# Kernel tuning notes

Hardware: AMD Instinct MI355X
Metric: run time of the kernel (lower is better)

The kernel has to match this reference:

```python
import jax, jax.numpy as jnp
import numpy as np

T, B, IN, OUT, N_MOD, K = 1024, 8, 1024, 1024, 16, 2

def setup_inputs() -> dict:
    key = jax.random.key(0)
    k1, k2, k3, k4 = jax.random.split(key, 4)
    x = jax.random.normal(k1, (T, B, IN), dtype=jnp.float32)
    selection = jax.random.randint(k2, (B, K), 0, N_MOD, dtype=jnp.int64)
    weight = jax.random.normal(k3, (N_MOD, IN, OUT), dtype=jnp.float32) * (1.0 / np.sqrt(IN))
    bias = jax.random.normal(k4, (N_MOD, OUT), dtype=jnp.float32) * 0.02
    return {"x": x, "selection": selection, "weight": weight, "bias": bias}

def reference(x, selection, weight, bias):
    # time_major=True: x is [T, B, in] -> batch-major [B, T, in]
    xb = jnp.swapaxes(x, 0, 1)
    # Gather the K selected expert weight matrices per batch row: [B, K, in, out]
    W_sel = weight[selection]
    # Equivalent to matmul(x[i], cat(weight[sel], dim=1)): [B, T, K, out]
    o = jnp.einsum('bti,bkio->btko', xb, W_sel)
    Bn, Tn, Kn, On = o.shape
    o = o.reshape(Bn, Tn, Kn * On)
    # concat_dim == 1 bias: bias[sel].view(1, -1) -> [1, K*out], broadcast over T
    o = o + bias[selection].reshape(Bn, 1, Kn * On)
    # back to time-major [T, B, K*out]
    return jnp.swapaxes(o, 0, 1)
```

## Files before the change

kernel.cpp:

```cpp
#include <hip/hip_runtime.h>

#define T_DIM 1024
#define B_DIM 8
#define IN_DIM 1024
#define OUT_DIM 1024
#define N_MODL 16
#define K_SEL 2

typedef unsigned short ushort_t;
typedef __bf16 bf16x8 __attribute__((ext_vector_type(8)));
typedef float f32x4 __attribute__((ext_vector_type(4)));

__device__ __forceinline__ unsigned int f2bf2(float lo, float hi) {
  union { float f; unsigned int u; } a, b; a.f = lo; b.f = hi;
  unsigned int ra = (a.u + 0x7fffu + ((a.u >> 16) & 1u)) >> 16;
  unsigned int rb = (b.u + 0x7fffu + ((b.u >> 16) & 1u)) >> 16;
  return ra | (rb << 16);
}

__device__ __forceinline__ void async_g2l(const void* g, void* l) {
  __builtin_amdgcn_global_load_lds(
      (const __attribute__((address_space(1))) unsigned int*)g,
      (__attribute__((address_space(3))) unsigned int*)l,
      16, 0, 0);
}

__device__ __forceinline__ int read_sel(const int* __restrict__ s, int g) {
  bool i64 = true;
#pragma unroll
  for (int j = 0; j < 8; ++j) i64 &= (s[2 * j + 1] == 0);
  return i64 ? s[2 * g] : s[g];
}

__global__ __launch_bounds__(256) void convert_kernel(const float* __restrict__ x,
                                                      const float* __restrict__ w,
                                                      const int* __restrict__ selp,
                                                      ushort_t* __restrict__ xb,
                                                      ushort_t* __restrict__ wt) {
  __shared__ ushort_t tb[128 * 128];
  const int bid = blockIdx.x;
  if (bid >= 1024) {
    const int i = (bid - 1024) * 256 + threadIdx.x;
    const float4* s = (const float4*)x;
    float4 a = s[i * 2], b = s[i * 2 + 1];
    uint4 o;
    o.x = f2bf2(a.x, a.y); o.y = f2bf2(a.z, a.w);
    o.z = f2bf2(b.x, b.y); o.w = f2bf2(b.z, b.w);
    ((uint4*)xb)[i] = o;
    return;
  }
  const int m = bid >> 6;
  bool used = false;
#pragma unroll
  for (int g = 0; g < B_DIM * K_SEL; ++g) used |= (read_sel(selp, g) == m);
  if (!used) return;

  const int i0 = ((bid >> 3) & 7) * 128;
  const int o0 = (bid & 7) * 128;
  const float* src = w + ((size_t)(m * IN_DIM + i0)) * OUT_DIM + o0;

  const int o4 = (threadIdx.x & 31) * 4;
  const int ib = threadIdx.x >> 5;
#pragma unroll
  for (int p = 0; p < 16; ++p) {
    const int i = ib + p * 8;
    float4 v = *(const float4*)(src + (size_t)i * OUT_DIM + o4);
    const int osw = o4 ^ (((i >> 3) & 15) << 2);
    uint2 d2; d2.x = f2bf2(v.x, v.y); d2.y = f2bf2(v.z, v.w);
    *(uint2*)(tb + i * 128 + osw) = d2;
  }
  __syncthreads();

  ushort_t* dst = wt + ((size_t)(m * OUT_DIM + o0)) * IN_DIM + i0;
  const int il = (threadIdx.x & 15) * 8;
  const int ob = threadIdx.x >> 4;
  const int q2 = ((il >> 3) & 15) << 2;
#pragma unroll
  for (int p = 0; p < 8; ++p) {
    const int o = ob + p * 16;
    const int osw = o ^ q2;
    uint4 d;
    unsigned int u[8];
#pragma unroll
    for (int j = 0; j < 8; ++j) u[j] = tb[(il + j) * 128 + osw];
    d.x = u[0] | (u[1] << 16); d.y = u[2] | (u[3] << 16);
    d.z = u[4] | (u[5] << 16); d.w = u[6] | (u[7] << 16);
    *(uint4*)(dst + (size_t)o * IN_DIM + il) = d;
  }
}

__global__ __launch_bounds__(256, 2) void mlgemm_kernel(const ushort_t* __restrict__ xb,
                                                        const ushort_t* __restrict__ wt,
                                                        const int* __restrict__ selp,
                                                        const float* __restrict__ bias,
                                                        float* __restrict__ out) {
  __shared__ ushort_t As[128 * 64];
  __shared__ ushort_t Bs[2][128 * 64];

  const int lin = blockIdx.x;
  const int b = lin & 7;
  const int mtile = (lin >> 3) & 7;
  const int ntile = lin >> 6;
  const int e0 = read_sel(selp, 2 * b);
  const int e1 = read_sel(selp, 2 * b + 1);

  const ushort_t* A  = xb + (size_t)b * IN_DIM;
  const ushort_t* B0 = wt + (size_t)e0 * OUT_DIM * IN_DIM;
  const ushort_t* B1 = wt + (size_t)e1 * OUT_DIM * IN_DIM;

  const int m0 = mtile * 128;
  const int n0 = ntile * 128;

  const int lane = threadIdx.x & 63;
  const int wv = threadIdx.x >> 6;

  const int srow = lane >> 3;
  const int sx = (((lane & 7) ^ (srow & 7)) << 3);
  const ushort_t* Ab  = A  + (size_t)(m0 + srow) * (B_DIM * IN_DIM) + sx;
  const ushort_t* Bb0 = B0 + (size_t)(n0 + srow) * IN_DIM + sx;
  const ushort_t* Bb1 = B1 + (size_t)(n0 + srow) * IN_DIM + sx;

  const int frow = lane & 15;
  const int quad = lane >> 4;
  const int cbase = ((quad ^ (frow & 7)) << 3);
  const int wrow = (wv & 1) * 64;
  const int wcol = (wv >> 1) * 64;
  const ushort_t* Ard  = As    + (wrow + frow) * 64;
  const ushort_t* Brd0 = Bs[0] + (wcol + frow) * 64;
  const ushort_t* Brd1 = Bs[1] + (wcol + frow) * 64;

  f32x4 acc0[4][4] = {};
  f32x4 acc1[4][4] = {};

  for (int k0 = 0; k0 < IN_DIM; k0 += 64) {
#pragma unroll
    for (int c = 0; c < 4; ++c) {
      const int j = wv * 4 + c;
      async_g2l(Ab  + (size_t)(8 * j) * (B_DIM * IN_DIM) + k0, As + j * 512);
      async_g2l(Bb0 + (size_t)(8 * j) * IN_DIM + k0, Bs[0] + j * 512);
      async_g2l(Bb1 + (size_t)(8 * j) * IN_DIM + k0, Bs[1] + j * 512);
    }
    __syncthreads();
#pragma unroll
    for (int kk = 0; kk < 64; kk += 32) {
      const int coff = cbase ^ kk;
      bf16x8 af[4], bf0[4], bf1[4];
#pragma unroll
      for (int i = 0; i < 4; ++i) {
        af[i]  = *(const bf16x8*)(Ard  + i * 16 * 64 + coff);
        bf0[i] = *(const bf16x8*)(Brd0 + i * 16 * 64 + coff);
        bf1[i] = *(const bf16x8*)(Brd1 + i * 16 * 64 + coff);
      }
#pragma unroll
      for (int mt = 0; mt < 4; ++mt)
#pragma unroll
        for (int nt = 0; nt < 4; ++nt) {
          acc0[mt][nt] = __builtin_amdgcn_mfma_f32_16x16x32_bf16(af[mt], bf0[nt],
                                                                 acc0[mt][nt], 0, 0, 0);
          acc1[mt][nt] = __builtin_amdgcn_mfma_f32_16x16x32_bf16(af[mt], bf1[nt],
                                                                 acc1[mt][nt], 0, 0, 0);
        }
    }
    __syncthreads();
  }

  const int orow0 = m0 + wrow + quad * 4;
  const int ocol0 = n0 + wcol + frow;
  const float* bp0 = bias + (size_t)e0 * OUT_DIM;
  const float* bp1 = bias + (size_t)e1 * OUT_DIM;
  float bv0[4], bv1[4];
#pragma unroll
  for (int nt = 0; nt < 4; ++nt) {
    bv0[nt] = bp0[ocol0 + nt * 16];
    bv1[nt] = bp1[ocol0 + nt * 16];
  }
  float* C0 = out + (size_t)b * (K_SEL * OUT_DIM);
  float* C1 = C0 + OUT_DIM;
#pragma unroll
  for (int mt = 0; mt < 4; ++mt) {
#pragma unroll
    for (int r = 0; r < 4; ++r) {
      const size_t rowoff = (size_t)(orow0 + mt * 16 + r) * (B_DIM * K_SEL * OUT_DIM);
#pragma unroll
      for (int nt = 0; nt < 4; ++nt) {
        C0[rowoff + ocol0 + nt * 16] = acc0[mt][nt][r] + bv0[nt];
        C1[rowoff + ocol0 + nt * 16] = acc1[mt][nt][r] + bv1[nt];
      }
    }
  }
}

extern "C" void kernel_launch(void* const* d_in, const int* in_sizes, int n_in,
                              void* d_out, int out_size, void* d_ws, size_t ws_size,
                              hipStream_t stream) {
  const float* x    = (const float*)d_in[0];
  const int*   sel  = (const int*)d_in[1];
  const float* w    = (const float*)d_in[2];
  const float* bias = (const float*)d_in[3];
  float* out = (float*)d_out;

  ushort_t* xb = (ushort_t*)d_ws;
  ushort_t* wt = (ushort_t*)((char*)d_ws +
                             (size_t)T_DIM * B_DIM * IN_DIM * 2);

  convert_kernel<<<dim3(1024 + T_DIM * B_DIM * IN_DIM / 8 / 256), 256, 0, stream>>>(
      x, w, sel, xb, wt);
  mlgemm_kernel<<<dim3(8 * 8 * B_DIM), 256, 0, stream>>>(xb, wt, sel, bias, out);
}
```

Measured before the change: 177.0 us.

## Rewrite expert GEMM with 256x256 tiles, double-buffered async LDS loads and MFMA priority

The grouped GEMM moves from 128x128 tiles covering both experts with 256 threads to 256x256 single-expert tiles with 512 threads (8 waves). Global-to-LDS loads are double-buffered and interleaved with MFMA phases using explicit s_barrier, waitcnt and sched_barrier, and s_setprio raises MFMA priority. The aim is to hide load latency and improve LDS reuse per tile. The grid shrinks to 256 blocks and LDS grows to 128KB per block, which lowers occupancy and may leave some compute units idle.

After: 177.4 us. No clear change (+0.2%).

```diff
diff --git a/kernel.cpp b/kernel.cpp
--- a/kernel.cpp
+++ b/kernel.cpp
@@ -89,103 +89,185 @@
   }
 }
 
-__global__ __launch_bounds__(256, 2) void mlgemm_kernel(const ushort_t* __restrict__ xb,
+#define MFMA16 __builtin_amdgcn_mfma_f32_16x16x32_bf16
+
+template<bool SN, bool SN2, bool WV, bool W0>
+__device__ __forceinline__ void gemm_step(
+    int s, ushort_t* curA, ushort_t* curB, ushort_t* nxtA, ushort_t* nxtB,
+    const ushort_t* aS, const ushort_t* bS, int stLds,
+    int ardo, int brdo, int cb, f32x4 (&acc)[8][4]) {
+  const int k0n  = (s + 1) << 6;
+  const int k0n2 = (s + 2) << 6;
+  const ushort_t* Ard = curA + ardo;
+  const ushort_t* Brd = curB + brdo;
+  bf16x8 bf0[4], bf1[4], af[4];
+
+#pragma unroll
+  for (int i = 0; i < 4; ++i) af[i] = *(const bf16x8*)(Ard + i * 1024 + cb);
+#pragma unroll
+  for (int n = 0; n < 4; ++n) bf0[n] = *(const bf16x8*)(Brd + n * 1024 + cb);
+  if (SN) async_g2l(aS + (size_t)64 * 8192 + k0n, nxtA + 4096 + stLds);
+  __builtin_amdgcn_sched_barrier(0);
+  __builtin_amdgcn_s_barrier();
+  asm volatile("s_waitcnt lgkmcnt(0)" ::: "memory");
+  __builtin_amdgcn_sched_barrier(0);
+  __builtin_amdgcn_s_setprio(1);
+#pragma unroll
+  for (int i = 0; i < 4; ++i)
+#pragma unroll
+    for (int n = 0; n < 4; ++n)
+      acc[i][n] = MFMA16(af[i], bf0[n], acc[i][n], 0, 0, 0);
+  __builtin_amdgcn_s_setprio(0);
+  __builtin_amdgcn_sched_barrier(0);
+  __builtin_amdgcn_s_barrier();
+
+#pragma unroll
+  for (int i = 0; i < 4; ++i) af[i] = *(const bf16x8*)(Ard + i * 1024 + (cb ^ 32));
+#pragma unroll
+  for (int n = 0; n < 4; ++n) bf1[n] = *(const bf16x8*)(Brd + n * 1024 + (cb ^ 32));
+  if (SN) async_g2l(aS + (size_t)192 * 8192 + k0n, nxtA + 3 * 4096 + stLds);
+  __builtin_amdgcn_sched_barrier(0);
+  __builtin_amdgcn_s_barrier();
+  asm volatile("s_waitcnt lgkmcnt(0)" ::: "memory");
+  __builtin_amdgcn_sched_barrier(0);
+  __builtin_amdgcn_s_setprio(1);
+#pragma unroll
+  for (int i = 0; i < 4; ++i)
+#pragma unroll
+    for (int n = 0; n < 4; ++n)
+      acc[i][n] = MFMA16(af[i], bf1[n], acc[i][n], 0, 0, 0);
+  __builtin_amdgcn_s_setprio(0);
+  __builtin_amdgcn_sched_barrier(0);
+  __builtin_amdgcn_s_barrier();
+
+#pragma unroll
+  for (int i = 0; i < 4; ++i) af[i] = *(const bf16x8*)(Ard + (4 + i) * 1024 + cb);
+  if (SN2) {
+    async_g2l(aS + k0n2,                      curA + stLds);
+    async_g2l(aS + (size_t)128 * 8192 + k0n2, curA + 2 * 4096 + stLds);
+    async_g2l(bS + k0n2,                      curB + stLds);
+    async_g2l(bS + (size_t)64 * 1024 + k0n2,  curB + 4096 + stLds);
+  }
+  __builtin_amdgcn_sched_barrier(0);
+  __builtin_amdgcn_s_barrier();
+  asm volatile("s_waitcnt lgkmcnt(0)" ::: "memory");
+  __builtin_amdgcn_sched_barrier(0);
+  __builtin_amdgcn_s_setprio(1);
+#pragma unroll
+  for (int i = 0; i < 4; ++i)
+#pragma unroll
+    for (int n = 0; n < 4; ++n)
+      acc[4 + i][n] = MFMA16(af[i], bf0[n], acc[4 + i][n], 0, 0, 0);
+  __builtin_amdgcn_s_setprio(0);
+  __builtin_amdgcn_sched_barrier(0);
+  __builtin_amdgcn_s_barrier();
+
+#pragma unroll
+  for (int i = 0; i < 4; ++i) af[i] = *(const bf16x8*)(Ard + (4 + i) * 1024 + (cb ^ 32));
+  if (SN2) {
+    async_g2l(bS + (size_t)128 * 1024 + k0n2, curB + 2 * 4096 + stLds);
+    async_g2l(bS + (size_t)192 * 1024 + k0n2, curB + 3 * 4096 + stLds);
+  }
+  __builtin_amdgcn_sched_barrier(0);
+  __builtin_amdgcn_s_barrier();
+  asm volatile("s_waitcnt lgkmcnt(0)" ::: "memory");
+  __builtin_amdgcn_sched_barrier(0);
+  __builtin_amdgcn_s_setprio(1);
+#pragma unroll
+  for (int i = 0; i < 4; ++i)
+#pragma unroll
+    for (int n = 0; n < 4; ++n)
+      acc[4 + i][n] = MFMA16(af[i], bf1[n], acc[4 + i][n], 0, 0, 0);
+  __builtin_amdgcn_s_setprio(0);
+  if (WV) {
+    if (W0) asm volatile("s_waitcnt vmcnt(0)" ::: "memory");
+    else    asm volatile("s_waitcnt vmcnt(6)" ::: "memory");
+  }
+  __builtin_amdgcn_sched_barrier(0);
+  __builtin_amdgcn_s_barrier();
+}
+
+__global__ __launch_bounds__(512, 2) void mlgemm_kernel(const ushort_t* __restrict__ xb,
                                                         const ushort_t* __restrict__ wt,
                                                         const int* __restrict__ selp,
                                                         const float* __restrict__ bias,
                                                         float* __restrict__ out) {
-  __shared__ ushort_t As[128 * 64];
-  __shared__ ushort_t Bs[2][128 * 64];
+  __shared__ ushort_t As[2][256 * 64];
+  __shared__ ushort_t Bs[2][256 * 64];
 
   const int lin = blockIdx.x;
   const int b = lin & 7;
-  const int mtile = (lin >> 3) & 7;
-  const int ntile = lin >> 6;
-  const int e0 = read_sel(selp, 2 * b);
-  const int e1 = read_sel(selp, 2 * b + 1);
-
-  const ushort_t* A  = xb + (size_t)b * IN_DIM;
-  const ushort_t* B0 = wt + (size_t)e0 * OUT_DIM * IN_DIM;
-  const ushort_t* B1 = wt + (size_t)e1 * OUT_DIM * IN_DIM;
-
-  const int m0 = mtile * 128;
-  const int n0 = ntile * 128;
-
-  const int lane = threadIdx.x & 63;
-  const int wv = threadIdx.x >> 6;
-
-  const int srow = lane >> 3;
-  const int sx = (((lane & 7) ^ (srow & 7)) << 3);
-  const ushort_t* Ab  = A  + (size_t)(m0 + srow) * (B_DIM * IN_DIM) + sx;
-  const ushort_t* Bb0 = B0 + (size_t)(n0 + srow) * IN_DIM + sx;
-  const ushort_t* Bb1 = B1 + (size_t)(n0 + srow) * IN_DIM + sx;
-
+  const int mtile = (lin >> 3) & 3;
+  const int ntile = lin >> 5;
+  const int e = (ntile < 4) ? read_sel(selp, 2 * b) : read_sel(selp, 2 * b + 1);
+  const int n0e = (ntile & 3) * 256;
+  const int m0 = mtile * 256;
+
+  const int tid = threadIdx.x;
+  const int lane = tid & 63;
+  const int wv = tid >> 6;
+  const int wm = wv >> 2;
+  const int wn = wv & 3;
   const int frow = lane & 15;
   const int quad = lane >> 4;
-  const int cbase = ((quad ^ (frow & 7)) << 3);
-  const int wrow = (wv & 1) * 64;
-  const int wcol = (wv >> 1) * 64;
-  const ushort_t* Ard  = As    + (wrow + frow) * 64;
-  const ushort_t* Brd0 = Bs[0] + (wcol + frow) * 64;
-  const ushort_t* Brd1 = Bs[1] + (wcol + frow) * 64;
-
-  f32x4 acc0[4][4] = {};
-  f32x4 acc1[4][4] = {};
-
-  for (int k0 = 0; k0 < IN_DIM; k0 += 64) {
-#pragma unroll
-    for (int c = 0; c < 4; ++c) {
-      const int j = wv * 4 + c;
-      async_g2l(Ab  + (size_t)(8 * j) * (B_DIM * IN_DIM) + k0, As + j * 512);
-      async_g2l(Bb0 + (size_t)(8 * j) * IN_DIM + k0, Bs[0] + j * 512);
-      async_g2l(Bb1 + (size_t)(8 * j) * IN_DIM + k0, Bs[1] + j * 512);
-    }
-    __syncthreads();
-#pragma unroll
-    for (int kk = 0; kk < 64; kk += 32) {
-      const int coff = cbase ^ kk;
-      bf16x8 af[4], bf0[4], bf1[4];
-#pragma unroll
-      for (int i = 0; i < 4; ++i) {
-        af[i]  = *(const bf16x8*)(Ard  + i * 16 * 64 + coff);
-        bf0[i] = *(const bf16x8*)(Brd0 + i * 16 * 64 + coff);
-        bf1[i] = *(const bf16x8*)(Brd1 + i * 16 * 64 + coff);
-      }
-#pragma unroll
-      for (int mt = 0; mt < 4; ++mt)
-#pragma unroll
-        for (int nt = 0; nt < 4; ++nt) {
-          acc0[mt][nt] = __builtin_amdgcn_mfma_f32_16x16x32_bf16(af[mt], bf0[nt],
-                                                                 acc0[mt][nt], 0, 0, 0);
-          acc1[mt][nt] = __builtin_amdgcn_mfma_f32_16x16x32_bf16(af[mt], bf1[nt],
-                                                                 acc1[mt][nt], 0, 0, 0);
-        }
-    }
-    __syncthreads();
-  }
-
-  const int orow0 = m0 + wrow + quad * 4;
-  const int ocol0 = n0 + wcol + frow;
-  const float* bp0 = bias + (size_t)e0 * OUT_DIM;
-  const float* bp1 = bias + (size_t)e1 * OUT_DIM;
-  float bv0[4], bv1[4];
-#pragma unroll
-  for (int nt = 0; nt < 4; ++nt) {
-    bv0[nt] = bp0[ocol0 + nt * 16];
-    bv1[nt] = bp1[ocol0 + nt * 16];
-  }
-  float* C0 = out + (size_t)b * (K_SEL * OUT_DIM);
-  float* C1 = C0 + OUT_DIM;
-#pragma unroll
-  for (int mt = 0; mt < 4; ++mt) {
+  const int cb = ((quad ^ (lane & 7)) << 3);
+
+  const int sr = tid >> 3;
+  const int sch = (tid & 7) ^ (sr & 7);
+  const ushort_t* aS = xb + (size_t)(m0 + sr) * (B_DIM * IN_DIM) + b * IN_DIM + sch * 8;
+  const ushort_t* bS = wt + ((size_t)(e * OUT_DIM + n0e + sr)) * IN_DIM + sch * 8;
+  const int stLds = wv * 512;
+
+  const int ardo = (wm * 128 + frow) * 64;
+  const int brdo = (wn * 64 + frow) * 64;
+
+  f32x4 acc[8][4] = {};
+
+  async_g2l(aS,                           As[0] + stLds);
+  async_g2l(aS + (size_t)64 * 8192,       As[0] + 4096 + stLds);
+  async_g2l(aS + (size_t)128 * 8192,      As[0] + 2 * 4096 + stLds);
+  async_g2l(aS + (size_t)192 * 8192,      As[0] + 3 * 4096 + stLds);
+  async_g2l(bS,                           Bs[0] + stLds);
+  async_g2l(bS + (size_t)64 * 1024,       Bs[0] + 4096 + stLds);
+  async_g2l(bS + (size_t)128 * 1024,      Bs[0] + 2 * 4096 + stLds);
+  async_g2l(bS + (size_t)192 * 1024,      Bs[0] + 3 * 4096 + stLds);
+  __builtin_amdgcn_sched_barrier(0);
+  async_g2l(aS + 64,                      As[1] + stLds);
+  async_g2l(aS + (size_t)128 * 8192 + 64, As[1] + 2 * 4096 + stLds);
+  async_g2l(bS + 64,                      Bs[1] + stLds);
+  async_g2l(bS + (size_t)64 * 1024 + 64,  Bs[1] + 4096 + stLds);
+  async_g2l(bS + (size_t)128 * 1024 + 64, Bs[1] + 2 * 4096 + stLds);
+  async_g2l(bS + (size_t)192 * 1024 + 64, Bs[1] + 3 * 4096 + stLds);
+  __builtin_amdgcn_sched_barrier(0);
+  asm volatile("s_waitcnt vmcnt(6)" ::: "memory");
+  __builtin_amdgcn_s_barrier();
+  __builtin_amdgcn_sched_barrier(0);
+
+  for (int s = 0; s < 14; s += 2) {
+    gemm_step<true, true, true, false>(s,     As[0], Bs[0], As[1], Bs[1],
+                                       aS, bS, stLds, ardo, brdo, cb, acc);
+    gemm_step<true, true, true, false>(s + 1, As[1], Bs[1], As[0], Bs[0],
+                                       aS, bS, stLds, ardo, brdo, cb, acc);
+  }
+  gemm_step<true, false, true, true>(14, As[0], Bs[0], As[1], Bs[1],
+                                     aS, bS, stLds, ardo, brdo, cb, acc);
+  gemm_step<false, false, false, false>(15, As[1], Bs[1], As[0], Bs[0],
+                                        aS, bS, stLds, ardo, brdo, cb, acc);
+
+  const float* bp = bias + (size_t)e * OUT_DIM + n0e + wn * 64 + frow;
+  float bv[4];
+#pragma unroll
+  for (int n = 0; n < 4; ++n) bv[n] = bp[n * 16];
+  const int colb = ntile * 256 + wn * 64 + frow;
+  const int trow = m0 + wm * 128 + quad * 4;
+  float* ob = out + (size_t)b * (K_SEL * OUT_DIM) + colb;
+#pragma unroll
+  for (int m = 0; m < 8; ++m) {
 #pragma unroll
     for (int r = 0; r < 4; ++r) {
-      const size_t rowoff = (size_t)(orow0 + mt * 16 + r) * (B_DIM * K_SEL * OUT_DIM);
-#pragma unroll
-      for (int nt = 0; nt < 4; ++nt) {
-        C0[rowoff + ocol0 + nt * 16] = acc0[mt][nt][r] + bv0[nt];
-        C1[rowoff + ocol0 + nt * 16] = acc1[mt][nt][r] + bv1[nt];
-      }
+      float* orow = ob + (size_t)(trow + m * 16 + r) * (B_DIM * K_SEL * OUT_DIM);
+#pragma unroll
+      for (int n = 0; n < 4; ++n) orow[n * 16] = acc[m][n][r] + bv[n];
     }
   }
 }
@@ -205,5 +287,5 @@
 
   convert_kernel<<<dim3(1024 + T_DIM * B_DIM * IN_DIM / 8 / 256), 256, 0, stream>>>(
       x, w, sel, xb, wt);
-  mlgemm_kernel<<<dim3(8 * 8 * B_DIM), 256, 0, stream>>>(xb, wt, sel, bias, out);
-}
+  mlgemm_kernel<<<dim3(8 * 4 * 8), 512, 0, stream>>>(xb, wt, sel, bias, out);
+}
```

## Triple-buffer LDS tiles with async prefetch two K-steps ahead

Applied to the files above, without the earlier changes.

Replaces the single-buffered 64-wide K loop with a three-stage ring of 32-wide LDS buffers. Global-to-LDS loads are issued two steps ahead, with manual vmcnt waits and one barrier per step, so memory latency overlaps the MFMA work. The LDS swizzle and load mapping are reworked for the narrower 32-element rows. In exchange there are more barriers and more manual waitcnt logic, and the changed swizzle could cause LDS bank conflicts.

Measured after the change: 179.5 us. Within noise of the previous version (+1.4%).

```diff
diff --git a/kernel.cpp b/kernel.cpp
--- a/kernel.cpp
+++ b/kernel.cpp
@@ -89,13 +89,15 @@
   }
 }
 
+#define MFMA16 __builtin_amdgcn_mfma_f32_16x16x32_bf16
+
 __global__ __launch_bounds__(256, 2) void mlgemm_kernel(const ushort_t* __restrict__ xb,
                                                         const ushort_t* __restrict__ wt,
                                                         const int* __restrict__ selp,
                                                         const float* __restrict__ bias,
                                                         float* __restrict__ out) {
-  __shared__ ushort_t As[128 * 64];
-  __shared__ ushort_t Bs[2][128 * 64];
+  __shared__ ushort_t As[3][128 * 32];
+  __shared__ ushort_t Bs[3][2][128 * 32];
 
   const int lin = blockIdx.x;
   const int b = lin & 7;
@@ -103,65 +105,94 @@
   const int ntile = lin >> 6;
   const int e0 = read_sel(selp, 2 * b);
   const int e1 = read_sel(selp, 2 * b + 1);
-
-  const ushort_t* A  = xb + (size_t)b * IN_DIM;
-  const ushort_t* B0 = wt + (size_t)e0 * OUT_DIM * IN_DIM;
-  const ushort_t* B1 = wt + (size_t)e1 * OUT_DIM * IN_DIM;
-
   const int m0 = mtile * 128;
   const int n0 = ntile * 128;
 
-  const int lane = threadIdx.x & 63;
-  const int wv = threadIdx.x >> 6;
-
-  const int srow = lane >> 3;
-  const int sx = (((lane & 7) ^ (srow & 7)) << 3);
-  const ushort_t* Ab  = A  + (size_t)(m0 + srow) * (B_DIM * IN_DIM) + sx;
-  const ushort_t* Bb0 = B0 + (size_t)(n0 + srow) * IN_DIM + sx;
-  const ushort_t* Bb1 = B1 + (size_t)(n0 + srow) * IN_DIM + sx;
+  const int tid = threadIdx.x;
+  const int lane = tid & 63;
+  const int wv = tid >> 6;
+
+  const int re = lane >> 2;
+  const int cl = (lane & 3) ^ ((lane >> 3) & 3);
+  const int j0 = wv * 2, j1 = j0 + 1;
+  const ushort_t* aP0 = xb + (size_t)(m0 + j0 * 16 + re) * (B_DIM * IN_DIM)
+                           + b * IN_DIM + cl * 8;
+  const ushort_t* aP1 = aP0 + (size_t)16 * (B_DIM * IN_DIM);
+  const ushort_t* b0P0 = wt + ((size_t)(e0 * OUT_DIM + n0 + j0 * 16 + re)) * IN_DIM
+                            + cl * 8;
+  const ushort_t* b0P1 = b0P0 + (size_t)16 * IN_DIM;
+  const ushort_t* b1P0 = wt + ((size_t)(e1 * OUT_DIM + n0 + j0 * 16 + re)) * IN_DIM
+                            + cl * 8;
+  const ushort_t* b1P1 = b1P0 + (size_t)16 * IN_DIM;
+  const int jo0 = j0 * 512, jo1 = j1 * 512;
 
   const int frow = lane & 15;
   const int quad = lane >> 4;
-  const int cbase = ((quad ^ (frow & 7)) << 3);
+  const int cp = quad ^ ((frow >> 1) & 3);
   const int wrow = (wv & 1) * 64;
   const int wcol = (wv >> 1) * 64;
-  const ushort_t* Ard  = As    + (wrow + frow) * 64;
-  const ushort_t* Brd0 = Bs[0] + (wcol + frow) * 64;
-  const ushort_t* Brd1 = Bs[1] + (wcol + frow) * 64;
+  const int rdoA = (wrow + frow) * 32 + cp * 8;
+  const int rdoB = (wcol + frow) * 32 + cp * 8;
 
   f32x4 acc0[4][4] = {};
   f32x4 acc1[4][4] = {};
 
-  for (int k0 = 0; k0 < IN_DIM; k0 += 64) {
-#pragma unroll
-    for (int c = 0; c < 4; ++c) {
-      const int j = wv * 4 + c;
-      async_g2l(Ab  + (size_t)(8 * j) * (B_DIM * IN_DIM) + k0, As + j * 512);
-      async_g2l(Bb0 + (size_t)(8 * j) * IN_DIM + k0, Bs[0] + j * 512);
-      async_g2l(Bb1 + (size_t)(8 * j) * IN_DIM + k0, Bs[1] + j * 512);
-    }
-    __syncthreads();
-#pragma unroll
-    for (int kk = 0; kk < 64; kk += 32) {
-      const int coff = cbase ^ kk;
-      bf16x8 af[4], bf0[4], bf1[4];
-#pragma unroll
-      for (int i = 0; i < 4; ++i) {
-        af[i]  = *(const bf16x8*)(Ard  + i * 16 * 64 + coff);
-        bf0[i] = *(const bf16x8*)(Brd0 + i * 16 * 64 + coff);
-        bf1[i] = *(const bf16x8*)(Brd1 + i * 16 * 64 + coff);
+#pragma unroll
+  for (int k = 0; k < 2; ++k) {
+    const int k0 = k * 32;
+    async_g2l(aP0 + k0,  As[k] + jo0);
+    async_g2l(aP1 + k0,  As[k] + jo1);
+    async_g2l(b0P0 + k0, Bs[k][0] + jo0);
+    async_g2l(b0P1 + k0, Bs[k][0] + jo1);
+    async_g2l(b1P0 + k0, Bs[k][1] + jo0);
+    async_g2l(b1P1 + k0, Bs[k][1] + jo1);
+  }
+  asm volatile("s_waitcnt vmcnt(6)" ::: "memory");
+  __builtin_amdgcn_sched_barrier(0);
+  __builtin_amdgcn_s_barrier();
+  __builtin_amdgcn_sched_barrier(0);
+
+#pragma unroll
+  for (int t = 0; t < 32; ++t) {
+    const int cur = t % 3;
+    const int nxt = (t + 2) % 3;
+    if (t < 30) {
+      const int k0n = (t + 2) * 32;
+      async_g2l(aP0 + k0n,  As[nxt] + jo0);
+      async_g2l(aP1 + k0n,  As[nxt] + jo1);
+      async_g2l(b0P0 + k0n, Bs[nxt][0] + jo0);
+      async_g2l(b0P1 + k0n, Bs[nxt][0] + jo1);
+      async_g2l(b1P0 + k0n, Bs[nxt][1] + jo0);
+      async_g2l(b1P1 + k0n, Bs[nxt][1] + jo1);
+      __builtin_amdgcn_sched_barrier(0);
+    }
+    const ushort_t* Ard  = As[cur] + rdoA;
+    const ushort_t* Brd0 = Bs[cur][0] + rdoB;
+    const ushort_t* Brd1 = Bs[cur][1] + rdoB;
+    bf16x8 af[4], bf0[4], bf1[4];
+#pragma unroll
+    for (int i = 0; i < 4; ++i) {
+      af[i]  = *(const bf16x8*)(Ard  + i * 512);
+      bf0[i] = *(const bf16x8*)(Brd0 + i * 512);
+      bf1[i] = *(const bf16x8*)(Brd1 + i * 512);
+    }
+#pragma unroll
+    for (int mt = 0; mt < 4; ++mt)
+#pragma unroll
+      for (int nt = 0; nt < 4; ++nt) {
+        acc0[mt][nt] = MFMA16(af[mt], bf0[nt], acc0[mt][nt], 0, 0, 0);
+        acc1[mt][nt] = MFMA16(af[mt], bf1[nt], acc1[mt][nt], 0, 0, 0);
       }
-#pragma unroll
-      for (int mt = 0; mt < 4; ++mt)
-#pragma unroll
-        for (int nt = 0; nt < 4; ++nt) {
-          acc0[mt][nt] = __builtin_amdgcn_mfma_f32_16x16x32_bf16(af[mt], bf0[nt],
-                                                                 acc0[mt][nt], 0, 0, 0);
-          acc1[mt][nt] = __builtin_amdgcn_mfma_f32_16x16x32_bf16(af[mt], bf1[nt],
-                                                                 acc1[mt][nt], 0, 0, 0);
-        }
-    }
-    __syncthreads();
+    if (t < 29) {
+      asm volatile("s_waitcnt vmcnt(6)" ::: "memory");
+    } else if (t < 31) {
+      asm volatile("s_waitcnt vmcnt(0)" ::: "memory");
+    }
+    if (t < 31) {
+      __builtin_amdgcn_sched_barrier(0);
+      __builtin_amdgcn_s_barrier();
+      __builtin_amdgcn_sched_barrier(0);
+    }
   }
 
   const int orow0 = m0 + wrow + quad * 4;
```

## Double-buffer B tiles and prefetch next k-step during MFMA compute

Applied to the files above, without the earlier changes.

Restructures the GEMM main loop into a software pipeline: the two expert weight tiles are double-buffered in LDS and the next k-step's B loads are issued before computing the current one. The A tile stays single-buffered and is reloaded right after its fragments are read into registers, behind a barrier. Manual waitcnt and sched_barrier calls control ordering. The goal is to hide global-to-LDS latency behind MFMA work, at the cost of 16KB more LDS (48KB per block), which may affect occupancy at 2 blocks per CU.

New measurement: 174.8 us. No clear change (-1.3%).

```diff
diff --git a/kernel.cpp b/kernel.cpp
--- a/kernel.cpp
+++ b/kernel.cpp
@@ -89,13 +89,89 @@
   }
 }
 
+#define MFMA16 __builtin_amdgcn_mfma_f32_16x16x32_bf16
+
+template<bool LAST>
+__device__ __forceinline__ void gstep(
+    int t, ushort_t* As,
+    const ushort_t* curB0, const ushort_t* curB1,
+    ushort_t* nxtB0, ushort_t* nxtB1,
+    const ushort_t* Ab, const ushort_t* Bb0, const ushort_t* Bb1,
+    int wv, int ardo, int brdo, int cb,
+    f32x4 (&acc0)[4][4], f32x4 (&acc1)[4][4]) {
+  const int k1 = (t + 1) * 64;
+  if (!LAST) {
+#pragma unroll
+    for (int c = 0; c < 4; ++c) {
+      const int j = wv * 4 + c;
+      async_g2l(Bb0 + (size_t)8 * j * IN_DIM + k1, nxtB0 + j * 512);
+      async_g2l(Bb1 + (size_t)8 * j * IN_DIM + k1, nxtB1 + j * 512);
+    }
+    __builtin_amdgcn_sched_barrier(0);
+  }
+  bf16x8 af0[4], af1[4];
+  const ushort_t* Ard = As + ardo;
+#pragma unroll
+  for (int i = 0; i < 4; ++i) {
+    af0[i] = *(const bf16x8*)(Ard + i * 1024 + cb);
+    af1[i] = *(const bf16x8*)(Ard + i * 1024 + (cb ^ 32));
+  }
+  if (!LAST) {
+    __builtin_amdgcn_sched_barrier(0);
+    asm volatile("s_waitcnt lgkmcnt(0)" ::: "memory");
+    __builtin_amdgcn_sched_barrier(0);
+    __builtin_amdgcn_s_barrier();
+    __builtin_amdgcn_sched_barrier(0);
+#pragma unroll
+    for (int c = 0; c < 4; ++c) {
+      const int j = wv * 4 + c;
+      async_g2l(Ab + (size_t)8 * j * (B_DIM * IN_DIM) + k1, As + j * 512);
+    }
+    __builtin_amdgcn_sched_barrier(0);
+  }
+  const ushort_t* Brd0 = curB0 + brdo;
+  const ushort_t* Brd1 = curB1 + brdo;
+  bf16x8 b0[4], b1[4];
+#pragma unroll
+  for (int n = 0; n < 4; ++n) {
+    b0[n] = *(const bf16x8*)(Brd0 + n * 1024 + cb);
+    b1[n] = *(const bf16x8*)(Brd1 + n * 1024 + cb);
+  }
+#pragma unroll
+  for (int mt = 0; mt < 4; ++mt)
+#pragma unroll
+    for (int nt = 0; nt < 4; ++nt) {
+      acc0[mt][nt] = MFMA16(af0[mt], b0[nt], acc0[mt][nt], 0, 0, 0);
+      acc1[mt][nt] = MFMA16(af0[mt], b1[nt], acc1[mt][nt], 0, 0, 0);
+    }
+#pragma unroll
+  for (int n = 0; n < 4; ++n) {
+    b0[n] = *(const bf16x8*)(Brd0 + n * 1024 + (cb ^ 32));
+    b1[n] = *(const bf16x8*)(Brd1 + n * 1024 + (cb ^ 32));
+  }
+#pragma unroll
+  for (int mt = 0; mt < 4; ++mt)
+#pragma unroll
+    for (int nt = 0; nt < 4; ++nt) {
+      acc0[mt][nt] = MFMA16(af1[mt], b0[nt], acc0[mt][nt], 0, 0, 0);
+      acc1[mt][nt] = MFMA16(af1[mt], b1[nt], acc1[mt][nt], 0, 0, 0);
+    }
+  if (!LAST) {
+    __builtin_amdgcn_sched_barrier(0);
+    asm volatile("s_waitcnt vmcnt(0)" ::: "memory");
+    __builtin_amdgcn_sched_barrier(0);
+    __builtin_amdgcn_s_barrier();
+    __builtin_amdgcn_sched_barrier(0);
+  }
+}
+
 __global__ __launch_bounds__(256, 2) void mlgemm_kernel(const ushort_t* __restrict__ xb,
                                                         const ushort_t* __restrict__ wt,
                                                         const int* __restrict__ selp,
                                                         const float* __restrict__ bias,
                                                         float* __restrict__ out) {
   __shared__ ushort_t As[128 * 64];
-  __shared__ ushort_t Bs[2][128 * 64];
+  __shared__ ushort_t Bs[2][2][128 * 64];
 
   const int lin = blockIdx.x;
   const int b = lin & 7;
@@ -103,11 +179,6 @@
   const int ntile = lin >> 6;
   const int e0 = read_sel(selp, 2 * b);
   const int e1 = read_sel(selp, 2 * b + 1);
-
-  const ushort_t* A  = xb + (size_t)b * IN_DIM;
-  const ushort_t* B0 = wt + (size_t)e0 * OUT_DIM * IN_DIM;
-  const ushort_t* B1 = wt + (size_t)e1 * OUT_DIM * IN_DIM;
-
   const int m0 = mtile * 128;
   const int n0 = ntile * 128;
 
@@ -116,53 +187,44 @@
 
   const int srow = lane >> 3;
   const int sx = (((lane & 7) ^ (srow & 7)) << 3);
-  const ushort_t* Ab  = A  + (size_t)(m0 + srow) * (B_DIM * IN_DIM) + sx;
-  const ushort_t* Bb0 = B0 + (size_t)(n0 + srow) * IN_DIM + sx;
-  const ushort_t* Bb1 = B1 + (size_t)(n0 + srow) * IN_DIM + sx;
+  const ushort_t* Ab  = xb + (size_t)(m0 + srow) * (B_DIM * IN_DIM) + b * IN_DIM + sx;
+  const ushort_t* Bb0 = wt + ((size_t)(e0 * OUT_DIM + n0 + srow)) * IN_DIM + sx;
+  const ushort_t* Bb1 = wt + ((size_t)(e1 * OUT_DIM + n0 + srow)) * IN_DIM + sx;
 
   const int frow = lane & 15;
   const int quad = lane >> 4;
-  const int cbase = ((quad ^ (frow & 7)) << 3);
+  const int cb = ((quad ^ (frow & 7)) << 3);
   const int wrow = (wv & 1) * 64;
   const int wcol = (wv >> 1) * 64;
-  const ushort_t* Ard  = As    + (wrow + frow) * 64;
-  const ushort_t* Brd0 = Bs[0] + (wcol + frow) * 64;
-  const ushort_t* Brd1 = Bs[1] + (wcol + frow) * 64;
+  const int ardo = (wrow + frow) * 64;
+  const int brdo = (wcol + frow) * 64;
 
   f32x4 acc0[4][4] = {};
   f32x4 acc1[4][4] = {};
 
-  for (int k0 = 0; k0 < IN_DIM; k0 += 64) {
-#pragma unroll
-    for (int c = 0; c < 4; ++c) {
-      const int j = wv * 4 + c;
-      async_g2l(Ab  + (size_t)(8 * j) * (B_DIM * IN_DIM) + k0, As + j * 512);
-      async_g2l(Bb0 + (size_t)(8 * j) * IN_DIM + k0, Bs[0] + j * 512);
-      async_g2l(Bb1 + (size_t)(8 * j) * IN_DIM + k0, Bs[1] + j * 512);
-    }
-    __syncthreads();
-#pragma unroll
-    for (int kk = 0; kk < 64; kk += 32) {
-      const int coff = cbase ^ kk;
-      bf16x8 af[4], bf0[4], bf1[4];
-#pragma unroll
-      for (int i = 0; i < 4; ++i) {
-        af[i]  = *(const bf16x8*)(Ard  + i * 16 * 64 + coff);
-        bf0[i] = *(const bf16x8*)(Brd0 + i * 16 * 64 + coff);
-        bf1[i] = *(const bf16x8*)(Brd1 + i * 16 * 64 + coff);
-      }
-#pragma unroll
-      for (int mt = 0; mt < 4; ++mt)
-#pragma unroll
-        for (int nt = 0; nt < 4; ++nt) {
-          acc0[mt][nt] = __builtin_amdgcn_mfma_f32_16x16x32_bf16(af[mt], bf0[nt],
-                                                                 acc0[mt][nt], 0, 0, 0);
-          acc1[mt][nt] = __builtin_amdgcn_mfma_f32_16x16x32_bf16(af[mt], bf1[nt],
-                                                                 acc1[mt][nt], 0, 0, 0);
-        }
-    }
-    __syncthreads();
-  }
+#pragma unroll
+  for (int c = 0; c < 4; ++c) {
+    const int j = wv * 4 + c;
+    async_g2l(Ab  + (size_t)8 * j * (B_DIM * IN_DIM), As + j * 512);
+    async_g2l(Bb0 + (size_t)8 * j * IN_DIM, Bs[0][0] + j * 512);
+    async_g2l(Bb1 + (size_t)8 * j * IN_DIM, Bs[0][1] + j * 512);
+  }
+  __builtin_amdgcn_sched_barrier(0);
+  asm volatile("s_waitcnt vmcnt(0)" ::: "memory");
+  __builtin_amdgcn_sched_barrier(0);
+  __builtin_amdgcn_s_barrier();
+  __builtin_amdgcn_sched_barrier(0);
+
+  for (int t = 0; t < 14; t += 2) {
+    gstep<false>(t,     As, Bs[0][0], Bs[0][1], Bs[1][0], Bs[1][1],
+                 Ab, Bb0, Bb1, wv, ardo, brdo, cb, acc0, acc1);
+    gstep<false>(t + 1, As, Bs[1][0], Bs[1][1], Bs[0][0], Bs[0][1],
+                 Ab, Bb0, Bb1, wv, ardo, brdo, cb, acc0, acc1);
+  }
+  gstep<false>(14, As, Bs[0][0], Bs[0][1], Bs[1][0], Bs[1][1],
+               Ab, Bb0, Bb1, wv, ardo, brdo, cb, acc0, acc1);
+  gstep<true>(15, As, Bs[1][0], Bs[1][1], Bs[0][0], Bs[0][1],
+              Ab, Bb0, Bb1, wv, ardo, brdo, cb, acc0, acc1);
 
   const int orow0 = m0 + wrow + quad * 4;
   const int ocol0 = n0 + wcol + frow;
```
